# Performance work log

Hardware: AMD Instinct MI355X
Metric: run time of the kernel (lower is better)

## Reference

```python
import jax, jax.numpy as jnp
import numpy as np

NUM_USERS = 80000
NUM_ITEMS = 40000
NUM_NODES = NUM_USERS + NUM_ITEMS
LATENT_DIM = 64
N_LAYERS = 3
ALPHA = 0.8
E_POS = 3_000_000
E_NEG = 1_500_000
E_PATH = 2_000_000
N_PATHS = 6


def _make_edges(rng, n_edges, n_nodes):
    # sample keys, dedupe so COO is coalesced (distinct (row,col) pairs)
    keys = rng.integers(0, n_nodes * n_nodes, size=int(n_edges * 1.05), dtype=np.int64)
    keys = np.unique(keys)[:n_edges]
    assert keys.shape[0] == n_edges
    row = (keys // n_nodes).astype(np.int32)
    col = (keys % n_nodes).astype(np.int32)
    return row, col


def setup_inputs() -> dict:
    key = jax.random.key(0)
    k1, k2, k3, k4, k5 = jax.random.split(key, 5)
    rng = np.random.default_rng(0)

    pos_row, pos_col = _make_edges(rng, E_POS, NUM_NODES)
    neg_row, neg_col = _make_edges(rng, E_NEG, NUM_NODES)
    p_row, p_col = _make_edges(rng, E_PATH, NUM_NODES)

    # path membership counts: for each coalesced edge, how many times each of the
    # 6 path matrices contains it (0/1 here); at least one path per edge
    counts = (rng.random((E_PATH, N_PATHS)) < 0.5).astype(np.float32)
    empty = counts.sum(axis=1) == 0
    counts[empty, 0] = 1.0

    return {
        "user_emb": 0.1 * jax.random.normal(k1, (NUM_USERS, LATENT_DIM), jnp.float32),
        "item_emb": 0.1 * jax.random.normal(k2, (NUM_ITEMS, LATENT_DIM), jnp.float32),
        "theta": jnp.ones((N_PATHS,), jnp.float32) / N_PATHS,
        "pos_row": jnp.asarray(pos_row),
        "pos_col": jnp.asarray(pos_col),
        "pos_val": jax.random.uniform(k3, (E_POS,), jnp.float32, 0.01, 1.0),
        "neg_row": jnp.asarray(neg_row),
        "neg_col": jnp.asarray(neg_col),
        "neg_val": jax.random.uniform(k4, (E_NEG,), jnp.float32, 0.01, 1.0),
        "p_row": jnp.asarray(p_row),
        "p_col": jnp.asarray(p_col),
        "p_counts": jnp.asarray(counts),
    }


def _spmm(row, col, val, x, n_nodes):
    # y = A @ x with A given as COO edge list: gather + segment scatter-add
    return jax.ops.segment_sum(val[:, None] * x[col], row, num_segments=n_nodes)


def reference(user_emb, item_emb, theta, pos_row, pos_col, pos_val,
              neg_row, neg_col, neg_val, p_row, p_col, p_counts):
    n = NUM_NODES

    # ---- build path-weighted matrix (coalesce + sparse row softmax, eq.(2)) ----
    theta_w = jax.nn.softmax(theta)                 # [6]
    vals = p_counts @ theta_w                       # coalesced values per edge [E_path]
    exp_v = jnp.exp(vals)
    row_sums = jax.ops.segment_sum(exp_v, p_row, num_segments=n)
    soft_v = exp_v / (row_sums[p_row] + 1e-12)      # row-level sparse softmax

    # ---- PEE: E_0 = P @ all_emb ----
    all_emb = jnp.concatenate([user_emb, item_emb], axis=0)  # [N, D]
    e = _spmm(p_row, p_col, soft_v, all_emb, n)
    embs = [e]

    # ---- signed propagation ----
    for _ in range(N_LAYERS):
        e_pos = _spmm(pos_row, pos_col, pos_val, e, n)
        e_neg_a = _spmm(neg_row, neg_col, neg_val, e, n)
        e = e_pos + ALPHA * (e - e_neg_a)
        embs.append(e)

    light_out = jnp.mean(jnp.stack(embs, axis=1), axis=1)   # [N, D]
    users = light_out[:NUM_USERS]
    items = light_out[NUM_USERS:]
    return users, items
```

## Files before the change

### kernel.cpp

```cpp
#include <hip/hip_runtime.h>

#define NUM_USERS 80000
#define NUM_ITEMS 40000
#define NUM_NODES 120000
#define DIM 64
#define ALPHA_C 0.8f

typedef unsigned short u16;
typedef unsigned int u32;

__device__ __forceinline__ u16 f2bf(float f) {
    union { float f; u32 i; } v;
    v.f = f;
    u32 i = v.i;
    u32 r = (i + 0x7FFFu + ((i >> 16) & 1u)) >> 16;
    return (u16)r;
}
__device__ __forceinline__ float lo_bf(u32 u) { return __uint_as_float(u << 16); }
__device__ __forceinline__ float hi_bf(u32 u) { return __uint_as_float(u & 0xffff0000u); }

__device__ __forceinline__ void acc8(float* __restrict__ acc, float v, uint4 q) {
    const u32* p = (const u32*)&q;
#pragma unroll
    for (int k = 0; k < 4; ++k) {
        u32 u = p[k];
        acc[2 * k]     = fmaf(v, lo_bf(u), acc[2 * k]);
        acc[2 * k + 1] = fmaf(v, hi_bf(u), acc[2 * k + 1]);
    }
}

__device__ __forceinline__ uint4 ldrow(const u16* __restrict__ x, int c, int li) {
    return *((const uint4*)(x + (size_t)c * DIM) + li);
}

template <bool SUMV>
__device__ __forceinline__ void seg_pipe_t(const int* __restrict__ col,
                                           const float* __restrict__ val,
                                           int start, int end,
                                           const u16* __restrict__ x,
                                           int li, float scale,
                                           float* __restrict__ acc,
                                           float* __restrict__ vsum) {
    int n = end - start;
    const int* cp = col + start;
    const float* vp = val + start;
    float s = 0.f;
    int np = n >> 1;
    if (np >= 2) {
        float va0 = vp[0], va1 = vp[1];
        int   cb0 = cp[2], cb1 = cp[3];
        float vb0 = vp[2], vb1 = vp[3];
        uint4 xa0 = ldrow(x, cp[0], li);
        uint4 xa1 = ldrow(x, cp[1], li);
        for (int p = 2; p < np; ++p) {
            int   cc0 = cp[2 * p],     cc1 = cp[2 * p + 1];
            float vc0 = vp[2 * p],     vc1 = vp[2 * p + 1];
            uint4 xb0 = ldrow(x, cb0, li);
            uint4 xb1 = ldrow(x, cb1, li);
            acc8(acc, va0 * scale, xa0);
            acc8(acc, va1 * scale, xa1);
            if (SUMV) s += va0 + va1;
            va0 = vb0; va1 = vb1; xa0 = xb0; xa1 = xb1;
            cb0 = cc0; cb1 = cc1; vb0 = vc0; vb1 = vc1;
        }
        uint4 xb0 = ldrow(x, cb0, li);
        uint4 xb1 = ldrow(x, cb1, li);
        acc8(acc, va0 * scale, xa0);
        acc8(acc, va1 * scale, xa1);
        acc8(acc, vb0 * scale, xb0);
        acc8(acc, vb1 * scale, xb1);
        if (SUMV) s += va0 + va1 + vb0 + vb1;
        if (n & 1) {
            float v = vp[n - 1];
            uint4 xq = ldrow(x, cp[n - 1], li);
            acc8(acc, v * scale, xq);
            if (SUMV) s += v;
        }
    } else {
        for (int e = 0; e < n; ++e) {
            float v = vp[e];
            uint4 xq = ldrow(x, cp[e], li);
            acc8(acc, v * scale, xq);
            if (SUMV) s += v;
        }
    }
    if (SUMV) *vsum = s;
}

__global__ void k_softmax_theta(const float* __restrict__ theta,
                                float* __restrict__ theta_w) {
    if (threadIdx.x == 0 && blockIdx.x == 0) {
        float m = -1e30f;
        for (int i = 0; i < 6; ++i) m = fmaxf(m, theta[i]);
        float e[6];
        float s = 0.f;
        for (int i = 0; i < 6; ++i) { e[i] = expf(theta[i] - m); s += e[i]; }
        for (int i = 0; i < 6; ++i) theta_w[i] = e[i] / s;
    }
}

__global__ void k_expv(const float* __restrict__ p_counts,
                       const float* __restrict__ theta_w,
                       float* __restrict__ exp_v, int E) {
    int i = blockIdx.x * blockDim.x + threadIdx.x;
    if (i >= E) return;
    const float* c = p_counts + (size_t)i * 6;
    float v = c[0] * theta_w[0] + c[1] * theta_w[1] + c[2] * theta_w[2] +
              c[3] * theta_w[3] + c[4] * theta_w[4] + c[5] * theta_w[5];
    exp_v[i] = expf(v);
}

__device__ __forceinline__ void lower_bound_ptr(const int* __restrict__ rows,
                                                int nnz, int r,
                                                int* __restrict__ ptr) {
    int lo = 0, hi = nnz;
    while (lo < hi) {
        int mid = (lo + hi) >> 1;
        if (rows[mid] < r) lo = mid + 1; else hi = mid;
    }
    ptr[r] = lo;
}

__global__ void k_row_ptr3(const int* __restrict__ rows_a, int nnz_a, int* __restrict__ pa,
                           const int* __restrict__ rows_b, int nnz_b, int* __restrict__ pb,
                           const int* __restrict__ rows_c, int nnz_c, int* __restrict__ pc) {
    int t = blockIdx.x * blockDim.x + threadIdx.x;
    int which = t / (NUM_NODES + 1);
    int r = t - which * (NUM_NODES + 1);
    if (which == 0) lower_bound_ptr(rows_a, nnz_a, r, pa);
    else if (which == 1) lower_bound_ptr(rows_b, nnz_b, r, pb);
    else if (which == 2) lower_bound_ptr(rows_c, nnz_c, r, pc);
}

__global__ void k_cvt(const float* __restrict__ user_emb,
                      const float* __restrict__ item_emb,
                      u16* __restrict__ emb16) {
    int i = blockIdx.x * blockDim.x + threadIdx.x;
    size_t f = (size_t)i * 4;
    const size_t UTOT = (size_t)NUM_USERS * DIM;
    const size_t TOT = (size_t)NUM_NODES * DIM;
    if (f >= TOT) return;
    float4 v = (f < UTOT) ? *(const float4*)(user_emb + f)
                          : *(const float4*)(item_emb + (f - UTOT));
    ushort4 o;
    o.x = f2bf(v.x); o.y = f2bf(v.y); o.z = f2bf(v.z); o.w = f2bf(v.w);
    *(ushort4*)(emb16 + f) = o;
}

__global__ void k_path(const u16* __restrict__ emb16,
                       const float* __restrict__ exp_v,
                       const int* __restrict__ rp,
                       const int* __restrict__ cols,
                       u16* __restrict__ e0) {
    int t = blockIdx.x * blockDim.x + threadIdx.x;
    int row = t >> 3;
    if (row >= NUM_NODES) return;
    int li = threadIdx.x & 7;
    int start = rp[row], end = rp[row + 1];

    float acc[8];
#pragma unroll
    for (int k = 0; k < 8; ++k) acc[k] = 0.f;
    float s = 0.f;

    seg_pipe_t<true>(cols, exp_v, start, end, emb16, li, 1.0f, acc, &s);

    float inv = 1.0f / (s + 1e-12f);
    u32 o[4];
#pragma unroll
    for (int k = 0; k < 4; ++k)
        o[k] = (u32)f2bf(acc[2 * k] * inv) | ((u32)f2bf(acc[2 * k + 1] * inv) << 16);
    *((uint4*)(e0 + (size_t)row * DIM) + li) = *(uint4*)o;
}

template <int FINAL>
__global__ void k_layer_t(const u16* __restrict__ e_in,
                          u16* __restrict__ e_out,
                          const u16* __restrict__ e0,
                          const u16* __restrict__ e1,
                          float* __restrict__ out,
                          const int* __restrict__ rp_p,
                          const int* __restrict__ col_p,
                          const float* __restrict__ val_p,
                          const int* __restrict__ rp_n,
                          const int* __restrict__ col_n,
                          const float* __restrict__ val_n) {
    int t = blockIdx.x * blockDim.x + threadIdx.x;
    int row = t >> 3;
    if (row >= NUM_NODES) return;
    int li = threadIdx.x & 7;

    uint4 eq = *((const uint4*)(e_in + (size_t)row * DIM) + li);

    float acc[8];
#pragma unroll
    for (int k = 0; k < 8; ++k) acc[k] = 0.f;

    seg_pipe_t<false>(col_p, val_p, rp_p[row], rp_p[row + 1], e_in, li, 1.0f,
                      acc, nullptr);
    seg_pipe_t<false>(col_n, val_n, rp_n[row], rp_n[row + 1], e_in, li, -ALPHA_C,
                      acc, nullptr);

    const u32* ep = (const u32*)&eq;
    float res[8];
#pragma unroll
    for (int k = 0; k < 4; ++k) {
        res[2 * k]     = acc[2 * k]     + ALPHA_C * lo_bf(ep[k]);
        res[2 * k + 1] = acc[2 * k + 1] + ALPHA_C * hi_bf(ep[k]);
    }

    if (FINAL) {
        uint4 q0 = *((const uint4*)(e0 + (size_t)row * DIM) + li);
        uint4 q1 = *((const uint4*)(e1 + (size_t)row * DIM) + li);
        const u32* p0 = (const u32*)&q0;
        const u32* p1 = (const u32*)&q1;
        float4 o0, o1;
        float* oo[2] = { (float*)&o0, (float*)&o1 };
#pragma unroll
        for (int k = 0; k < 4; ++k) {
            float lo = res[2 * k]     + lo_bf(ep[k]) + lo_bf(p0[k]) + lo_bf(p1[k]);
            float hi = res[2 * k + 1] + hi_bf(ep[k]) + hi_bf(p0[k]) + hi_bf(p1[k]);
            oo[k >> 1][(k & 1) * 2]     = 0.25f * lo;
            oo[k >> 1][(k & 1) * 2 + 1] = 0.25f * hi;
        }
        float4* sp = (float4*)(out + (size_t)row * DIM) + li * 2;
        sp[0] = o0;
        sp[1] = o1;
    } else {
        u32 o[4];
#pragma unroll
        for (int k = 0; k < 4; ++k)
            o[k] = (u32)f2bf(res[2 * k]) | ((u32)f2bf(res[2 * k + 1]) << 16);
        *((uint4*)(e_out + (size_t)row * DIM) + li) = *(uint4*)o;
    }
}

extern "C" void kernel_launch(void* const* d_in, const int* in_sizes, int n_in,
                              void* d_out, int out_size, void* d_ws, size_t ws_size,
                              hipStream_t stream) {
    const float* user_emb = (const float*)d_in[0];
    const float* item_emb = (const float*)d_in[1];
    const float* theta    = (const float*)d_in[2];
    const int*   pos_row  = (const int*)d_in[3];
    const int*   pos_col  = (const int*)d_in[4];
    const float* pos_val  = (const float*)d_in[5];
    const int*   neg_row  = (const int*)d_in[6];
    const int*   neg_col  = (const int*)d_in[7];
    const float* neg_val  = (const float*)d_in[8];
    const int*   p_row    = (const int*)d_in[9];
    const int*   p_col    = (const int*)d_in[10];
    const float* p_counts = (const float*)d_in[11];
    const int E_pos  = in_sizes[3];
    const int E_neg  = in_sizes[6];
    const int E_path = in_sizes[9];

    char* wsb = (char*)d_ws;
    size_t off = 0;
    auto alloc = [&](size_t bytes) -> void* {
        void* p = wsb + off;
        off = (off + bytes + 255) & ~(size_t)255;
        return p;
    };
    float* theta_w = (float*)alloc(6 * sizeof(float));
    float* exp_v   = (float*)alloc((size_t)E_path * sizeof(float));
    int*   rp_pos  = (int*)alloc((size_t)(NUM_NODES + 1) * sizeof(int));
    int*   rp_neg  = (int*)alloc((size_t)(NUM_NODES + 1) * sizeof(int));
    int*   rp_path = (int*)alloc((size_t)(NUM_NODES + 1) * sizeof(int));
    u16*   emb16   = (u16*)alloc((size_t)NUM_NODES * DIM * sizeof(u16));
    u16*   e0      = (u16*)alloc((size_t)NUM_NODES * DIM * sizeof(u16));
    u16*   e1      = (u16*)alloc((size_t)NUM_NODES * DIM * sizeof(u16));
    u16*   e2      = (u16*)alloc((size_t)NUM_NODES * DIM * sizeof(u16));
    float* outp    = (float*)d_out;

    k_softmax_theta<<<1, 64, 0, stream>>>(theta, theta_w);
    k_expv<<<(E_path + 255) / 256, 256, 0, stream>>>(p_counts, theta_w, exp_v, E_path);

    int total_rp = 3 * (NUM_NODES + 1);
    k_row_ptr3<<<(total_rp + 255) / 256, 256, 0, stream>>>(
        pos_row, E_pos, rp_pos, neg_row, E_neg, rp_neg, p_row, E_path, rp_path);

    int cvt_threads = (NUM_NODES * DIM) / 4;
    k_cvt<<<(cvt_threads + 255) / 256, 256, 0, stream>>>(user_emb, item_emb, emb16);

    int row_blocks = (NUM_NODES + 31) / 32;

    k_path<<<row_blocks, 256, 0, stream>>>(emb16, exp_v, rp_path, p_col, e0);
    k_layer_t<0><<<row_blocks, 256, 0, stream>>>(e0, e1, nullptr, nullptr, nullptr,
                                                 rp_pos, pos_col, pos_val,
                                                 rp_neg, neg_col, neg_val);
    k_layer_t<0><<<row_blocks, 256, 0, stream>>>(e1, e2, nullptr, nullptr, nullptr,
                                                 rp_pos, pos_col, pos_val,
                                                 rp_neg, neg_col, neg_val);
    k_layer_t<1><<<row_blocks, 256, 0, stream>>>(e2, nullptr, e0, e1, outp,
                                                 rp_pos, pos_col, pos_val,
                                                 rp_neg, neg_col, neg_val);
}
```

Before: 461.0 us.

## Merge pos/neg CSR into packed col-val edge list and deepen gather pipeline

Adds a preprocessing kernel that interleaves positive and negative edges per row into one packed (col, value) int2 array, folding the -alpha scale into the negative values. Each propagation layer then walks a single merged segment with 8-byte loads instead of two segments with separate column and value arrays. The gather pipeline is deepened from two to four edge-pairs in flight, and nontemporal stores and loads are used for the outputs. The e2 buffer now reuses emb16. This costs one extra pass over all signed edges plus the workspace for the merged array, which is amortised across the three layers.

```diff
diff --git a/kernel.cpp b/kernel.cpp
--- a/kernel.cpp
+++ b/kernel.cpp
@@ -8,6 +8,9 @@
 
 typedef unsigned short u16;
 typedef unsigned int u32;
+typedef int   i2v __attribute__((ext_vector_type(2)));
+typedef u32   u4v __attribute__((ext_vector_type(4)));
+typedef float f4v __attribute__((ext_vector_type(4)));
 
 __device__ __forceinline__ u16 f2bf(float f) {
     union { float f; u32 i; } v;
@@ -33,54 +36,80 @@
     return *((const uint4*)(x + (size_t)c * DIM) + li);
 }
 
-template <bool SUMV>
-__device__ __forceinline__ void seg_pipe_t(const int* __restrict__ col,
-                                           const float* __restrict__ val,
-                                           int start, int end,
-                                           const u16* __restrict__ x,
-                                           int li, float scale,
-                                           float* __restrict__ acc,
-                                           float* __restrict__ vsum) {
-    int n = end - start;
-    const int* cp = col + start;
-    const float* vp = val + start;
+template <bool SUMV, bool PACKED>
+__device__ __forceinline__ void seg_pipe(const int* __restrict__ cp0,
+                                         const float* __restrict__ vp0,
+                                         const i2v* __restrict__ ep0,
+                                         int start, int end,
+                                         const u16* __restrict__ x,
+                                         int li,
+                                         float* __restrict__ acc,
+                                         float* __restrict__ vsum) {
+    const int n = end - start;
+    const int* cp = nullptr;
+    const float* vp = nullptr;
+    const i2v* ep = nullptr;
+    if constexpr (PACKED) { ep = ep0 + start; }
+    else { cp = cp0 + start; vp = vp0 + start; }
+
+    auto LDE = [&](int i, int& c, float& v) {
+        if constexpr (PACKED) {
+            i2v e = ep[i];
+            c = e.x;
+            v = __int_as_float(e.y);
+        } else {
+            c = cp[i];
+            v = vp[i];
+        }
+    };
+
     float s = 0.f;
-    int np = n >> 1;
-    if (np >= 2) {
-        float va0 = vp[0], va1 = vp[1];
-        int   cb0 = cp[2], cb1 = cp[3];
-        float vb0 = vp[2], vb1 = vp[3];
-        uint4 xa0 = ldrow(x, cp[0], li);
-        uint4 xa1 = ldrow(x, cp[1], li);
-        for (int p = 2; p < np; ++p) {
-            int   cc0 = cp[2 * p],     cc1 = cp[2 * p + 1];
-            float vc0 = vp[2 * p],     vc1 = vp[2 * p + 1];
-            uint4 xb0 = ldrow(x, cb0, li);
-            uint4 xb1 = ldrow(x, cb1, li);
-            acc8(acc, va0 * scale, xa0);
-            acc8(acc, va1 * scale, xa1);
+    const int np = n >> 1;
+    if (np >= 4) {
+        int ca0, ca1, cb0, cb1, cc0, cc1, cd0, cd1;
+        float va0, va1, vb0, vb1, vc0, vc1, vd0, vd1;
+        LDE(0, ca0, va0); LDE(1, ca1, va1);
+        LDE(2, cb0, vb0); LDE(3, cb1, vb1);
+        LDE(4, cc0, vc0); LDE(5, cc1, vc1);
+        LDE(6, cd0, vd0); LDE(7, cd1, vd1);
+        uint4 xa0 = ldrow(x, ca0, li), xa1 = ldrow(x, ca1, li);
+        uint4 xb0 = ldrow(x, cb0, li), xb1 = ldrow(x, cb1, li);
+        for (int p = 4; p < np; ++p) {
+            int ce0, ce1; float ve0, ve1;
+            LDE(2 * p, ce0, ve0); LDE(2 * p + 1, ce1, ve1);
+            uint4 xc0 = ldrow(x, cc0, li);
+            uint4 xc1 = ldrow(x, cc1, li);
+            acc8(acc, va0, xa0);
+            acc8(acc, va1, xa1);
             if (SUMV) s += va0 + va1;
-            va0 = vb0; va1 = vb1; xa0 = xb0; xa1 = xb1;
-            cb0 = cc0; cb1 = cc1; vb0 = vc0; vb1 = vc1;
-        }
-        uint4 xb0 = ldrow(x, cb0, li);
-        uint4 xb1 = ldrow(x, cb1, li);
-        acc8(acc, va0 * scale, xa0);
-        acc8(acc, va1 * scale, xa1);
-        acc8(acc, vb0 * scale, xb0);
-        acc8(acc, vb1 * scale, xb1);
-        if (SUMV) s += va0 + va1 + vb0 + vb1;
+            va0 = vb0; va1 = vb1; vb0 = vc0; vb1 = vc1; vc0 = vd0; vc1 = vd1;
+            vd0 = ve0; vd1 = ve1;
+            cc0 = cd0; cc1 = cd1; cd0 = ce0; cd1 = ce1;
+            xa0 = xb0; xa1 = xb1; xb0 = xc0; xb1 = xc1;
+        }
+        uint4 xc0 = ldrow(x, cc0, li), xc1 = ldrow(x, cc1, li);
+        uint4 xd0 = ldrow(x, cd0, li), xd1 = ldrow(x, cd1, li);
+        acc8(acc, va0, xa0); acc8(acc, va1, xa1);
+        if (SUMV) s += va0 + va1;
+        acc8(acc, vb0, xb0); acc8(acc, vb1, xb1);
+        if (SUMV) s += vb0 + vb1;
+        acc8(acc, vc0, xc0); acc8(acc, vc1, xc1);
+        if (SUMV) s += vc0 + vc1;
+        acc8(acc, vd0, xd0); acc8(acc, vd1, xd1);
+        if (SUMV) s += vd0 + vd1;
         if (n & 1) {
-            float v = vp[n - 1];
-            uint4 xq = ldrow(x, cp[n - 1], li);
-            acc8(acc, v * scale, xq);
+            int c; float v;
+            LDE(n - 1, c, v);
+            uint4 xq = ldrow(x, c, li);
+            acc8(acc, v, xq);
             if (SUMV) s += v;
         }
     } else {
         for (int e = 0; e < n; ++e) {
-            float v = vp[e];
-            uint4 xq = ldrow(x, cp[e], li);
-            acc8(acc, v * scale, xq);
+            int c; float v;
+            LDE(e, c, v);
+            uint4 xq = ldrow(x, c, li);
+            acc8(acc, v, xq);
             if (SUMV) s += v;
         }
     }
@@ -147,6 +176,38 @@
     *(ushort4*)(emb16 + f) = o;
 }
 
+__global__ void k_merge(const int* __restrict__ rp_p, const int* __restrict__ col_p,
+                        const float* __restrict__ val_p,
+                        const int* __restrict__ rp_n, const int* __restrict__ col_n,
+                        const float* __restrict__ val_n,
+                        i2v* __restrict__ mev, int* __restrict__ rp_m,
+                        int nnz_total) {
+    int t = blockIdx.x * blockDim.x + threadIdx.x;
+    int row = t >> 3;
+    if (row >= NUM_NODES) return;
+    int li = threadIdx.x & 7;
+    int sp = rp_p[row], np = rp_p[row + 1] - sp;
+    int sn = rp_n[row], nn = rp_n[row + 1] - sn;
+    int base = sp + sn;
+    if (li == 0) {
+        rp_m[row] = base;
+        if (row == 0) rp_m[NUM_NODES] = nnz_total;
+    }
+    for (int i = li; i < np; i += 8) {
+        i2v e;
+        e.x = __builtin_nontemporal_load(col_p + sp + i);
+        e.y = __float_as_int(__builtin_nontemporal_load(val_p + sp + i));
+        __builtin_nontemporal_store(e, mev + base + i);
+    }
+    int b2 = base + np;
+    for (int i = li; i < nn; i += 8) {
+        i2v e;
+        e.x = __builtin_nontemporal_load(col_n + sn + i);
+        e.y = __float_as_int(-ALPHA_C * __builtin_nontemporal_load(val_n + sn + i));
+        __builtin_nontemporal_store(e, mev + b2 + i);
+    }
+}
+
 __global__ void k_path(const u16* __restrict__ emb16,
                        const float* __restrict__ exp_v,
                        const int* __restrict__ rp,
@@ -163,14 +224,15 @@
     for (int k = 0; k < 8; ++k) acc[k] = 0.f;
     float s = 0.f;
 
-    seg_pipe_t<true>(cols, exp_v, start, end, emb16, li, 1.0f, acc, &s);
+    seg_pipe<true, false>(cols, exp_v, nullptr, start, end, emb16, li, acc, &s);
 
     float inv = 1.0f / (s + 1e-12f);
     u32 o[4];
 #pragma unroll
     for (int k = 0; k < 4; ++k)
         o[k] = (u32)f2bf(acc[2 * k] * inv) | ((u32)f2bf(acc[2 * k + 1] * inv) << 16);
-    *((uint4*)(e0 + (size_t)row * DIM) + li) = *(uint4*)o;
+    u4v vv; vv.x = o[0]; vv.y = o[1]; vv.z = o[2]; vv.w = o[3];
+    __builtin_nontemporal_store(vv, (u4v*)(e0 + (size_t)row * DIM) + li);
 }
 
 template <int FINAL>
@@ -179,59 +241,53 @@
                           const u16* __restrict__ e0,
                           const u16* __restrict__ e1,
                           float* __restrict__ out,
-                          const int* __restrict__ rp_p,
-                          const int* __restrict__ col_p,
-                          const float* __restrict__ val_p,
-                          const int* __restrict__ rp_n,
-                          const int* __restrict__ col_n,
-                          const float* __restrict__ val_n) {
+                          const int* __restrict__ rp_m,
+                          const i2v* __restrict__ mev) {
     int t = blockIdx.x * blockDim.x + threadIdx.x;
     int row = t >> 3;
     if (row >= NUM_NODES) return;
     int li = threadIdx.x & 7;
 
+    float acc[8];
+#pragma unroll
+    for (int k = 0; k < 8; ++k) acc[k] = 0.f;
+
+    seg_pipe<false, true>(nullptr, nullptr, mev, rp_m[row], rp_m[row + 1],
+                          e_in, li, acc, nullptr);
+
     uint4 eq = *((const uint4*)(e_in + (size_t)row * DIM) + li);
-
-    float acc[8];
-#pragma unroll
-    for (int k = 0; k < 8; ++k) acc[k] = 0.f;
-
-    seg_pipe_t<false>(col_p, val_p, rp_p[row], rp_p[row + 1], e_in, li, 1.0f,
-                      acc, nullptr);
-    seg_pipe_t<false>(col_n, val_n, rp_n[row], rp_n[row + 1], e_in, li, -ALPHA_C,
-                      acc, nullptr);
-
-    const u32* ep = (const u32*)&eq;
+    const u32* ep_ = (const u32*)&eq;
     float res[8];
 #pragma unroll
     for (int k = 0; k < 4; ++k) {
-        res[2 * k]     = acc[2 * k]     + ALPHA_C * lo_bf(ep[k]);
-        res[2 * k + 1] = acc[2 * k + 1] + ALPHA_C * hi_bf(ep[k]);
+        res[2 * k]     = acc[2 * k]     + ALPHA_C * lo_bf(ep_[k]);
+        res[2 * k + 1] = acc[2 * k + 1] + ALPHA_C * hi_bf(ep_[k]);
     }
 
     if (FINAL) {
-        uint4 q0 = *((const uint4*)(e0 + (size_t)row * DIM) + li);
-        uint4 q1 = *((const uint4*)(e1 + (size_t)row * DIM) + li);
-        const u32* p0 = (const u32*)&q0;
-        const u32* p1 = (const u32*)&q1;
-        float4 o0, o1;
-        float* oo[2] = { (float*)&o0, (float*)&o1 };
+        u4v q0 = __builtin_nontemporal_load((const u4v*)(e0 + (size_t)row * DIM) + li);
+        u4v q1 = __builtin_nontemporal_load((const u4v*)(e1 + (size_t)row * DIM) + li);
+        float of[8];
 #pragma unroll
         for (int k = 0; k < 4; ++k) {
-            float lo = res[2 * k]     + lo_bf(ep[k]) + lo_bf(p0[k]) + lo_bf(p1[k]);
-            float hi = res[2 * k + 1] + hi_bf(ep[k]) + hi_bf(p0[k]) + hi_bf(p1[k]);
-            oo[k >> 1][(k & 1) * 2]     = 0.25f * lo;
-            oo[k >> 1][(k & 1) * 2 + 1] = 0.25f * hi;
-        }
-        float4* sp = (float4*)(out + (size_t)row * DIM) + li * 2;
-        sp[0] = o0;
-        sp[1] = o1;
+            float lo = res[2 * k]     + lo_bf(ep_[k]) + lo_bf(q0[k]) + lo_bf(q1[k]);
+            float hi = res[2 * k + 1] + hi_bf(ep_[k]) + hi_bf(q0[k]) + hi_bf(q1[k]);
+            of[2 * k]     = 0.25f * lo;
+            of[2 * k + 1] = 0.25f * hi;
+        }
+        f4v o0, o1;
+        o0.x = of[0]; o0.y = of[1]; o0.z = of[2]; o0.w = of[3];
+        o1.x = of[4]; o1.y = of[5]; o1.z = of[6]; o1.w = of[7];
+        f4v* sp = (f4v*)(out + (size_t)row * DIM) + li * 2;
+        __builtin_nontemporal_store(o0, sp);
+        __builtin_nontemporal_store(o1, sp + 1);
     } else {
         u32 o[4];
 #pragma unroll
         for (int k = 0; k < 4; ++k)
             o[k] = (u32)f2bf(res[2 * k]) | ((u32)f2bf(res[2 * k + 1]) << 16);
-        *((uint4*)(e_out + (size_t)row * DIM) + li) = *(uint4*)o;
+        u4v vv; vv.x = o[0]; vv.y = o[1]; vv.z = o[2]; vv.w = o[3];
+        __builtin_nontemporal_store(vv, (u4v*)(e_out + (size_t)row * DIM) + li);
     }
 }
 
@@ -266,10 +322,12 @@
     int*   rp_pos  = (int*)alloc((size_t)(NUM_NODES + 1) * sizeof(int));
     int*   rp_neg  = (int*)alloc((size_t)(NUM_NODES + 1) * sizeof(int));
     int*   rp_path = (int*)alloc((size_t)(NUM_NODES + 1) * sizeof(int));
+    int*   rp_m    = (int*)alloc((size_t)(NUM_NODES + 1) * sizeof(int));
+    i2v*   mev     = (i2v*)alloc((size_t)(E_pos + E_neg) * sizeof(i2v));
     u16*   emb16   = (u16*)alloc((size_t)NUM_NODES * DIM * sizeof(u16));
     u16*   e0      = (u16*)alloc((size_t)NUM_NODES * DIM * sizeof(u16));
     u16*   e1      = (u16*)alloc((size_t)NUM_NODES * DIM * sizeof(u16));
-    u16*   e2      = (u16*)alloc((size_t)NUM_NODES * DIM * sizeof(u16));
+    u16*   e2      = emb16;
     float* outp    = (float*)d_out;
 
     k_softmax_theta<<<1, 64, 0, stream>>>(theta, theta_w);
@@ -284,14 +342,15 @@
 
     int row_blocks = (NUM_NODES + 31) / 32;
 
+    k_merge<<<row_blocks, 256, 0, stream>>>(rp_pos, pos_col, pos_val,
+                                            rp_neg, neg_col, neg_val,
+                                            mev, rp_m, E_pos + E_neg);
+
     k_path<<<row_blocks, 256, 0, stream>>>(emb16, exp_v, rp_path, p_col, e0);
     k_layer_t<0><<<row_blocks, 256, 0, stream>>>(e0, e1, nullptr, nullptr, nullptr,
-                                                 rp_pos, pos_col, pos_val,
-                                                 rp_neg, neg_col, neg_val);
+                                                 rp_m, mev);
     k_layer_t<0><<<row_blocks, 256, 0, stream>>>(e1, e2, nullptr, nullptr, nullptr,
-                                                 rp_pos, pos_col, pos_val,
-                                                 rp_neg, neg_col, neg_val);
+                                                 rp_m, mev);
     k_layer_t<1><<<row_blocks, 256, 0, stream>>>(e2, nullptr, e0, e1, outp,
-                                                 rp_pos, pos_col, pos_val,
-                                                 rp_neg, neg_col, neg_val);
-}
+                                                 rp_m, mev);
+}
```

New measurement: 492.8 us. 1.07x slower.
